# Optimization experiments

Hardware: AMD Instinct MI355X
Metric: run time of the kernel (lower is better)

## Reference

```python
import jax, jax.numpy as jnp
import numpy as np

N_NODES = 20000
N_EDGES = 8192
UNITS = 128
NUM_GAUSSIANS = 50
CUTOFF = 8.0
GAMMA = 10.0
MIN_DIST, MAX_DIST = 0.0, 30.0


def setup_inputs() -> dict:
    key = jax.random.key(0)
    ks = jax.random.split(key, 6)
    node_features = jax.random.normal(ks[0], (N_NODES, UNITS), dtype=jnp.float32)
    edge_indices = jax.random.randint(ks[1], (2, N_EDGES), 0, N_NODES, dtype=jnp.int32)
    distances = jax.random.uniform(ks[2], (N_EDGES,), dtype=jnp.float32)
    # filter network params (Dense(units) -> swish -> Dense(units*units))
    W1 = jax.random.normal(ks[3], (NUM_GAUSSIANS, UNITS), dtype=jnp.float32) / np.sqrt(NUM_GAUSSIANS)
    b1 = jnp.zeros((UNITS,), dtype=jnp.float32)
    W2 = jax.random.normal(ks[4], (UNITS, UNITS * UNITS), dtype=jnp.float32) / np.sqrt(UNITS)
    b2 = jnp.zeros((UNITS * UNITS,), dtype=jnp.float32)
    # transform Dense(units, use_bias=False)
    Wt = jax.random.normal(ks[5], (UNITS, UNITS), dtype=jnp.float32) / np.sqrt(UNITS)
    return {"node_features": node_features, "edge_indices": edge_indices,
            "distances": distances, "W1": W1, "b1": b1, "W2": W2, "b2": b2, "Wt": Wt}


def reference(node_features, edge_indices, distances, W1, b1, W2, b2, Wt):
    n_nodes, units = node_features.shape
    # cutoff mask (multiplicative; dropped edges contribute zero to the scatter-sum,
    # equivalent to tf.boolean_mask + unsorted_segment_sum)
    mask = (distances <= CUTOFF).astype(node_features.dtype)  # [E]
    # Gaussian basis expansion
    centers = jnp.linspace(MIN_DIST, MAX_DIST, NUM_GAUSSIANS, dtype=jnp.float32)
    df = jnp.exp(-GAMMA * jnp.square(distances[:, None] - centers[None, :]))  # [E, G]
    # filter network: Dense -> swish -> Dense(units*units)
    h = jax.nn.silu(df @ W1 + b1)                    # [E, U]
    filters = (h @ W2 + b2).reshape(-1, units, units)  # [E, U, U]
    # gather source node features, transform, per-edge matvec
    src = node_features[edge_indices[0]]             # [E, U]
    transformed = src @ Wt                           # [E, U]
    filtered = jnp.einsum('eij,ej->ei', filters, transformed) * mask[:, None]  # [E, U]
    # scatter-sum to destination nodes
    messages = jax.ops.segment_sum(filtered, edge_indices[1], num_segments=n_nodes)
    return jax.nn.silu(messages)
```

## Files before the change

kernel.cpp:

```cpp
#include <hip/hip_runtime.h>
#include <hip/hip_fp16.h>


typedef _Float16 f16;
typedef __attribute__((ext_vector_type(8))) f16 f16x8;
typedef __attribute__((ext_vector_type(4))) float f32x4;
typedef __attribute__((ext_vector_type(4))) unsigned int u32x4;

#define NEDGE 8192
#define NNODE 20000
#define NG    50
#define KSTEPS 516
#define W2C_BYTES (KSTEPS * 8192)
#define HT_ROWS 132
#define HT_BYTES (HT_ROWS * 8192 * 2)
#define TM_BYTES (NEDGE * 128 * 2)

#define LDS_H   0
#define LDS_TM  5120
#define LDS_B   37888
#define LDS_TOT 70656

static __device__ __forceinline__ float fsilu(float x) { return x / (1.0f + __expf(-x)); }

static __device__ __forceinline__ void gll16(const void* g, void* l) {
  __builtin_amdgcn_global_load_lds(
      (const __attribute__((address_space(1))) unsigned int*)g,
      (__attribute__((address_space(3))) unsigned int*)l, 16, 0, 0);
}

__global__ __launch_bounds__(256) void k0_w2c(const float* __restrict__ W2,
                                              const float* __restrict__ b2,
                                              f16* __restrict__ w2c) {
  int gidx = blockIdx.x * 256 + threadIdx.x;
  int lane = gidx & 63;
  int nt   = (gidx >> 6) & 7;
  int step = gidx >> 9;
  int k0i = step * 32 + (lane >> 4) * 8;
  int i   = nt * 16 + (lane & 15);
  int u   = k0i >> 7, j0 = k0i & 127;
  const float* src = (u < 128) ? (W2 + (size_t)u * 16384 + i * 128 + j0)
                               : (b2 + i * 128 + j0);
  union { f16 s[8]; u32x4 v; } pk;
#pragma unroll
  for (int r = 0; r < 8; ++r) pk.s[r] = (f16)src[r];
  *((u32x4*)w2c + gidx) = pk.v;
}

__global__ __launch_bounds__(256) void k1_edge(const float* __restrict__ NF,
                                               const int*   __restrict__ EI,
                                               const float* __restrict__ DI,
                                               const float* __restrict__ W1,
                                               const float* __restrict__ B1,
                                               const float* __restrict__ WT,
                                               f16* __restrict__ ht,
                                               f16* __restrict__ tmo) {
  __shared__ float df[16][NG];
  __shared__ float s_mask[16];
  __shared__ float s_src[16][128];
  __shared__ float t_tile[16][132];
  __shared__ float h_tile[16][132];
  int et = blockIdx.x, e0 = et * 16, tid = threadIdx.x;

  for (int idx = tid; idx < 16 * NG; idx += 256) {
    int e = idx / NG, g = idx - e * NG;
    float d = DI[e0 + e];
    float x = d - (float)g * (30.0f / 49.0f);
    df[e][g] = __expf(-10.0f * x * x);
  }
  if (tid < 16) s_mask[tid] = (DI[e0 + tid] <= 8.0f) ? 1.0f : 0.0f;
  for (int idx = tid; idx < 16 * 128; idx += 256) {
    int e = idx >> 7, u = idx & 127;
    s_src[e][u] = NF[(size_t)EI[e0 + e] * 128 + u];
  }
  __syncthreads();

  int j = tid & 127, es = tid >> 7;
  for (int e = es * 8; e < es * 8 + 8; ++e) {
    float acc = B1[j];
    for (int g = 0; g < NG; ++g) acc += df[e][g] * W1[g * 128 + j];
    h_tile[e][j] = fsilu(acc);
  }
  {
    float acc[8] = {0.f,0.f,0.f,0.f,0.f,0.f,0.f,0.f};
    for (int u = 0; u < 128; ++u) {
      float wv = WT[u * 128 + j];
#pragma unroll
      for (int e8 = 0; e8 < 8; ++e8) acc[e8] += s_src[es * 8 + e8][u] * wv;
    }
#pragma unroll
    for (int e8 = 0; e8 < 8; ++e8) t_tile[es * 8 + e8][j] = acc[e8];
  }
  __syncthreads();

  {
    int u = tid >> 1, hf = tid & 1;
    union { f16 s[8]; u32x4 v; } pk;
#pragma unroll
    for (int k = 0; k < 8; ++k) pk.s[k] = (f16)h_tile[hf * 8 + k][u];
    *(u32x4*)(ht + (size_t)u * 8192 + e0 + hf * 8) = pk.v;
  }
  if (tid < 16) ht[(size_t)128 * 8192 + e0 + tid] = (f16)1.0f;
  {
    int e = tid >> 4, cc = tid & 15;
    float m = s_mask[e];
    union { f16 s[8]; u32x4 v; } pk;
#pragma unroll
    for (int k = 0; k < 8; ++k) pk.s[k] = (f16)(m * t_tile[e][cc * 8 + k]);
    *(u32x4*)(tmo + (size_t)(e0 + e) * 128 + cc * 8) = pk.v;
  }
}

__global__ __launch_bounds__(256, 2) void k2_gemm(const f16* __restrict__ w2c,
                                                  const f16* __restrict__ ht,
                                                  const f16* __restrict__ tm,
                                                  const int* __restrict__ EI,
                                                  float* __restrict__ msg) {
  __shared__ u32x4 smem_v[LDS_TOT / 16];
  char* smem = (char*)smem_v;

  int bid = blockIdx.x;
  int c   = bid & 7;
  int eb  = bid >> 3;
  int e0  = eb * 128;
  int u0  = c * 16;
  int gstep0 = c * 64;
  int nsteps = (c == 7) ? 68 : 64;
  int tid = threadIdx.x, w = tid >> 6, lane = tid & 63;
  int l15 = lane & 15, g4 = lane >> 4;

  if (w == 0) {
#pragma unroll
    for (int q = 0; q < 5; ++q) {
      const char* src = (const char*)ht + ((size_t)(u0 + q * 4 + g4) * 8192 + e0 + l15 * 8) * 2;
      gll16(src, smem + LDS_H + q * 1024 + lane * 16);
    }
  }
#pragma unroll
  for (int it = 0; it < 8; ++it) {
    int ck = it * 256 + tid;
    int e = ck >> 4, jc = ck & 15;
    u32x4 v = *(const u32x4*)((const char*)tm + (size_t)(e0 + e) * 256 + jc * 16);
    *(u32x4*)(smem + LDS_TM + e * 256 + ((jc * 16) ^ ((e & 7) << 4))) = v;
  }
  const char* bsrc = (const char*)w2c + (size_t)gstep0 * 8192;
#pragma unroll
  for (int q = 0; q < 4; ++q)
    gll16(bsrc + w * 4096 + q * 1024 + lane * 16,
          smem + LDS_B + w * 4096 + q * 1024 + lane * 16);
  asm volatile("s_waitcnt vmcnt(0)" ::: "memory");
  __syncthreads();

  f32x4 acc[2][8];
#pragma unroll
  for (int rt = 0; rt < 2; ++rt)
#pragma unroll
    for (int nt = 0; nt < 8; ++nt) acc[rt][nt] = (f32x4){0.f, 0.f, 0.f, 0.f};

  __half2 hb0 = __half2half2(__half(0.f)), hb1 = hb0;
  const int tmswz = (l15 & 7) << 4;
  const int tma0  = LDS_TM + (w * 32 + l15) * 256;
  int nph = nsteps >> 1;

  for (int ph = 0; ph < nph; ++ph) {
    int cur = ph & 1;
    if (ph + 1 < nph) {
      const char* ns = bsrc + (size_t)(ph + 1) * 16384;
#pragma unroll
      for (int q = 0; q < 4; ++q)
        gll16(ns + w * 4096 + q * 1024 + lane * 16,
              smem + LDS_B + (1 - cur) * 16384 + w * 4096 + q * 1024 + lane * 16);
    }
    if ((ph & 1) == 0) {
      int uu = ph >> 1;
      const __half* hrow = (const __half*)(smem + LDS_H + uu * 256);
      hb0 = __half2half2(hrow[w * 32 + l15]);
      hb1 = __half2half2(hrow[w * 32 + 16 + l15]);
    }
#pragma unroll
    for (int s = 0; s < 2; ++s) {
      int s4 = ((ph & 1) << 1) | s;
      int coloff = (s4 * 64 + g4 * 16) ^ tmswz;
      union { f16x8 v; __half2 h2[4]; } t0, t1, a0, a1;
      t0.v = *(const f16x8*)(smem + tma0 + coloff);
      t1.v = *(const f16x8*)(smem + tma0 + 4096 + coloff);
#pragma unroll
      for (int q = 0; q < 4; ++q) {
        a0.h2[q] = __hmul2(t0.h2[q], hb0);
        a1.h2[q] = __hmul2(t1.h2[q], hb1);
      }
      const char* bb = smem + LDS_B + cur * 16384 + s * 8192 + lane * 16;
#pragma unroll
      for (int nt = 0; nt < 8; ++nt) {
        f16x8 b = *(const f16x8*)(bb + nt * 1024);
        acc[0][nt] = __builtin_amdgcn_mfma_f32_16x16x32_f16(a0.v, b, acc[0][nt], 0, 0, 0);
        acc[1][nt] = __builtin_amdgcn_mfma_f32_16x16x32_f16(a1.v, b, acc[1][nt], 0, 0, 0);
      }
    }
    asm volatile("s_waitcnt vmcnt(0)" ::: "memory");
    __syncthreads();
  }

  const int* dst = EI + NEDGE;
  int erow = e0 + w * 32;
#pragma unroll
  for (int rt = 0; rt < 2; ++rt)
#pragma unroll
    for (int r = 0; r < 4; ++r) {
      int e = erow + rt * 16 + g4 * 4 + r;
      float* row = msg + (size_t)dst[e] * 128 + l15;
#pragma unroll
      for (int nt = 0; nt < 8; ++nt)
        atomicAdd(row + nt * 16, acc[rt][nt][r]);
    }
}

__global__ __launch_bounds__(256) void k3_silu(float* __restrict__ out, int n4) {
  int idx = blockIdx.x * 256 + threadIdx.x;
  int stride = gridDim.x * 256;
  f32x4* p = (f32x4*)out;
  for (; idx < n4; idx += stride) {
    f32x4 v = p[idx];
#pragma unroll
    for (int cc = 0; cc < 4; ++cc) v[cc] = fsilu(v[cc]);
    p[idx] = v;
  }
}

extern "C" void kernel_launch(void* const* d_in, const int* in_sizes, int n_in,
                              void* d_out, int out_size, void* d_ws, size_t ws_size,
                              hipStream_t stream) {
  const float* NF = (const float*)d_in[0];
  const int*   EI = (const int*)  d_in[1];
  const float* DI = (const float*)d_in[2];
  const float* W1 = (const float*)d_in[3];
  const float* B1 = (const float*)d_in[4];
  const float* W2 = (const float*)d_in[5];
  const float* B2 = (const float*)d_in[6];
  const float* WT = (const float*)d_in[7];
  float* out = (float*)d_out;

  f16* w2c = (f16*)d_ws;
  f16* ht  = (f16*)((char*)d_ws + W2C_BYTES);
  f16* tmo = (f16*)((char*)d_ws + W2C_BYTES + HT_BYTES);
  size_t needed = (size_t)W2C_BYTES + HT_BYTES + TM_BYTES;
  if (ws_size < needed) return;

  hipMemsetAsync(d_out, 0, (size_t)out_size * sizeof(float), stream);
  k0_w2c <<<dim3(1032), dim3(256), 0, stream>>>(W2, B2, w2c);
  k1_edge<<<dim3(512),  dim3(256), 0, stream>>>(NF, EI, DI, W1, B1, WT, ht, tmo);
  k2_gemm<<<dim3(512),  dim3(256), 0, stream>>>(w2c, ht, tmo, EI, out);
  k3_silu<<<dim3(1024), dim3(256), 0, stream>>>(out, out_size / 4);
}
```

Baseline: 95.61 us.

## Restructure GEMM to 2x2 wave tiling with 4-stage B pipeline and pre-swizzled inputs

The edge kernel now writes the h matrix blocked per 128-edge tile and stores transformed features already XOR-swizzled, so the GEMM kernel can load both with direct global-to-LDS copies instead of register round-trips. The GEMM changes from a 1x4 wave layout (32 rows x 128 cols per wave) to a 2x2 layout (64x64 per wave), which cuts LDS reads per MFMA. It also replaces double buffering with a 4-slot ring and a partial vmcnt wait, so loads run further ahead without draining the queue each step. MFMA sections are wrapped in setprio. The deeper ring and larger A footprint raise register use, which may affect occupancy.

```diff
diff --git a/kernel.cpp b/kernel.cpp
--- a/kernel.cpp
+++ b/kernel.cpp
@@ -12,8 +12,7 @@
 #define NG    50
 #define KSTEPS 516
 #define W2C_BYTES (KSTEPS * 8192)
-#define HT_ROWS 132
-#define HT_BYTES (HT_ROWS * 8192 * 2)
+#define HT_BYTES (64 * 132 * 128 * 2)
 #define TM_BYTES (NEDGE * 128 * 2)
 
 #define LDS_H   0
@@ -53,7 +52,7 @@
                                                const float* __restrict__ W1,
                                                const float* __restrict__ B1,
                                                const float* __restrict__ WT,
-                                               f16* __restrict__ ht,
+                                               f16* __restrict__ ht2,
                                                f16* __restrict__ tmo) {
   __shared__ float df[16][NG];
   __shared__ float s_mask[16];
@@ -93,126 +92,130 @@
   }
   __syncthreads();
 
+  int eb = et >> 3, el0 = (et & 7) * 16;
   {
     int u = tid >> 1, hf = tid & 1;
     union { f16 s[8]; u32x4 v; } pk;
 #pragma unroll
     for (int k = 0; k < 8; ++k) pk.s[k] = (f16)h_tile[hf * 8 + k][u];
-    *(u32x4*)(ht + (size_t)u * 8192 + e0 + hf * 8) = pk.v;
-  }
-  if (tid < 16) ht[(size_t)128 * 8192 + e0 + tid] = (f16)1.0f;
+    *(u32x4*)(ht2 + ((size_t)eb * 132 + u) * 128 + el0 + hf * 8) = pk.v;
+  }
+  if (tid < 16) ht2[((size_t)eb * 132 + 128) * 128 + el0 + tid] = (f16)1.0f;
   {
     int e = tid >> 4, cc = tid & 15;
     float m = s_mask[e];
     union { f16 s[8]; u32x4 v; } pk;
 #pragma unroll
     for (int k = 0; k < 8; ++k) pk.s[k] = (f16)(m * t_tile[e][cc * 8 + k]);
-    *(u32x4*)(tmo + (size_t)(e0 + e) * 128 + cc * 8) = pk.v;
+    int col = (cc * 16) ^ ((e & 7) << 4);
+    *(u32x4*)((char*)tmo + (size_t)(e0 + e) * 256 + col) = pk.v;
   }
 }
 
 __global__ __launch_bounds__(256, 2) void k2_gemm(const f16* __restrict__ w2c,
-                                                  const f16* __restrict__ ht,
+                                                  const f16* __restrict__ ht2,
                                                   const f16* __restrict__ tm,
                                                   const int* __restrict__ EI,
                                                   float* __restrict__ msg) {
   __shared__ u32x4 smem_v[LDS_TOT / 16];
   char* smem = (char*)smem_v;
 
-  int bid = blockIdx.x;
-  int c   = bid & 7;
-  int eb  = bid >> 3;
-  int e0  = eb * 128;
-  int u0  = c * 16;
-  int gstep0 = c * 64;
-  int nsteps = (c == 7) ? 68 : 64;
-  int tid = threadIdx.x, w = tid >> 6, lane = tid & 63;
-  int l15 = lane & 15, g4 = lane >> 4;
-
+  const int bid = blockIdx.x;
+  const int c   = bid & 7;
+  const int eb  = bid >> 3;
+  const int e0  = eb * 128;
+  const int nu  = (c == 7) ? 17 : 16;
+  const int nph = nu * 4;
+  const int tid = threadIdx.x, w = tid >> 6, lane = tid & 63;
+  const int l15 = lane & 15, g4 = lane >> 4;
+  const int wm = w >> 1, wn = w & 1;
+
+  const char* bsrc = (const char*)w2c + (size_t)(c * 64) * 8192;
+
+  {
+    const char* tsrc = (const char*)tm + (size_t)e0 * 256 + w * 8192;
+#pragma unroll
+    for (int q = 0; q < 8; ++q)
+      gll16(tsrc + q * 1024 + lane * 16,
+            smem + LDS_TM + w * 8192 + q * 1024 + lane * 16);
+  }
   if (w == 0) {
-#pragma unroll
-    for (int q = 0; q < 5; ++q) {
-      const char* src = (const char*)ht + ((size_t)(u0 + q * 4 + g4) * 8192 + e0 + l15 * 8) * 2;
-      gll16(src, smem + LDS_H + q * 1024 + lane * 16);
+    const char* hsrc = (const char*)ht2 + ((size_t)eb * 132 + c * 16) * 256;
+#pragma unroll
+    for (int q = 0; q < 5; ++q)
+      gll16(hsrc + q * 1024 + lane * 16, smem + LDS_H + q * 1024 + lane * 16);
+  }
+#pragma unroll
+  for (int q = 0; q < 2; ++q)
+    gll16(bsrc + w * 2048 + q * 1024 + lane * 16,
+          smem + LDS_B + w * 2048 + q * 1024 + lane * 16);
+#pragma unroll
+  for (int q = 0; q < 2; ++q)
+    gll16(bsrc + 8192 + w * 2048 + q * 1024 + lane * 16,
+          smem + LDS_B + 8192 + w * 2048 + q * 1024 + lane * 16);
+  asm volatile("s_waitcnt vmcnt(2)" ::: "memory");
+  __builtin_amdgcn_s_barrier();
+
+  f32x4 acc[4][4];
+#pragma unroll
+  for (int rt = 0; rt < 4; ++rt)
+#pragma unroll
+    for (int nt = 0; nt < 4; ++nt) acc[rt][nt] = (f32x4){0.f, 0.f, 0.f, 0.f};
+
+  const int tmbase = LDS_TM + (wm * 64 + l15) * 256;
+  const int colsw  = (l15 & 7) << 4;
+  const int bcol   = wn * 4096 + lane * 16;
+  const __half* hbase = (const __half*)(smem + LDS_H) + wm * 64 + l15;
+
+  for (int u = 0; u < nu; ++u) {
+    __half2 h2[4];
+#pragma unroll
+    for (int rt = 0; rt < 4; ++rt) h2[rt] = __half2half2(hbase[u * 128 + rt * 16]);
+#pragma unroll
+    for (int jc = 0; jc < 4; ++jc) {
+      const int p = u * 4 + jc;
+      int ps = p + 2; ps = (ps < nph) ? ps : (nph - 1);
+      const char* ns = bsrc + (size_t)ps * 8192 + w * 2048;
+      char* nd = smem + LDS_B + ((jc + 2) & 3) * 8192 + w * 2048;
+      gll16(ns + lane * 16, nd + lane * 16);
+      gll16(ns + 1024 + lane * 16, nd + 1024 + lane * 16);
+      union uf { f16x8 v; __half2 h[4]; };
+      uf a[4];
+#pragma unroll
+      for (int rt = 0; rt < 4; ++rt) {
+        uf t;
+        t.v = *(const f16x8*)(smem + tmbase + rt * 4096 + ((jc * 64 + g4 * 16) ^ colsw));
+#pragma unroll
+        for (int q = 0; q < 4; ++q) a[rt].h[q] = __hmul2(t.h[q], h2[rt]);
+      }
+      f16x8 b[4];
+#pragma unroll
+      for (int nt = 0; nt < 4; ++nt)
+        b[nt] = *(const f16x8*)(smem + LDS_B + jc * 8192 + bcol + nt * 1024);
+      __builtin_amdgcn_s_setprio(1);
+#pragma unroll
+      for (int nt = 0; nt < 4; ++nt)
+#pragma unroll
+        for (int rt = 0; rt < 4; ++rt)
+          acc[rt][nt] = __builtin_amdgcn_mfma_f32_16x16x32_f16(a[rt].v, b[nt], acc[rt][nt], 0, 0, 0);
+      __builtin_amdgcn_s_setprio(0);
+      asm volatile("s_waitcnt vmcnt(2)" ::: "memory");
+      __builtin_amdgcn_s_barrier();
     }
   }
-#pragma unroll
-  for (int it = 0; it < 8; ++it) {
-    int ck = it * 256 + tid;
-    int e = ck >> 4, jc = ck & 15;
-    u32x4 v = *(const u32x4*)((const char*)tm + (size_t)(e0 + e) * 256 + jc * 16);
-    *(u32x4*)(smem + LDS_TM + e * 256 + ((jc * 16) ^ ((e & 7) << 4))) = v;
-  }
-  const char* bsrc = (const char*)w2c + (size_t)gstep0 * 8192;
-#pragma unroll
-  for (int q = 0; q < 4; ++q)
-    gll16(bsrc + w * 4096 + q * 1024 + lane * 16,
-          smem + LDS_B + w * 4096 + q * 1024 + lane * 16);
-  asm volatile("s_waitcnt vmcnt(0)" ::: "memory");
-  __syncthreads();
-
-  f32x4 acc[2][8];
-#pragma unroll
-  for (int rt = 0; rt < 2; ++rt)
-#pragma unroll
-    for (int nt = 0; nt < 8; ++nt) acc[rt][nt] = (f32x4){0.f, 0.f, 0.f, 0.f};
-
-  __half2 hb0 = __half2half2(__half(0.f)), hb1 = hb0;
-  const int tmswz = (l15 & 7) << 4;
-  const int tma0  = LDS_TM + (w * 32 + l15) * 256;
-  int nph = nsteps >> 1;
-
-  for (int ph = 0; ph < nph; ++ph) {
-    int cur = ph & 1;
-    if (ph + 1 < nph) {
-      const char* ns = bsrc + (size_t)(ph + 1) * 16384;
-#pragma unroll
-      for (int q = 0; q < 4; ++q)
-        gll16(ns + w * 4096 + q * 1024 + lane * 16,
-              smem + LDS_B + (1 - cur) * 16384 + w * 4096 + q * 1024 + lane * 16);
-    }
-    if ((ph & 1) == 0) {
-      int uu = ph >> 1;
-      const __half* hrow = (const __half*)(smem + LDS_H + uu * 256);
-      hb0 = __half2half2(hrow[w * 32 + l15]);
-      hb1 = __half2half2(hrow[w * 32 + 16 + l15]);
-    }
-#pragma unroll
-    for (int s = 0; s < 2; ++s) {
-      int s4 = ((ph & 1) << 1) | s;
-      int coloff = (s4 * 64 + g4 * 16) ^ tmswz;
-      union { f16x8 v; __half2 h2[4]; } t0, t1, a0, a1;
-      t0.v = *(const f16x8*)(smem + tma0 + coloff);
-      t1.v = *(const f16x8*)(smem + tma0 + 4096 + coloff);
-#pragma unroll
-      for (int q = 0; q < 4; ++q) {
-        a0.h2[q] = __hmul2(t0.h2[q], hb0);
-        a1.h2[q] = __hmul2(t1.h2[q], hb1);
-      }
-      const char* bb = smem + LDS_B + cur * 16384 + s * 8192 + lane * 16;
-#pragma unroll
-      for (int nt = 0; nt < 8; ++nt) {
-        f16x8 b = *(const f16x8*)(bb + nt * 1024);
-        acc[0][nt] = __builtin_amdgcn_mfma_f32_16x16x32_f16(a0.v, b, acc[0][nt], 0, 0, 0);
-        acc[1][nt] = __builtin_amdgcn_mfma_f32_16x16x32_f16(a1.v, b, acc[1][nt], 0, 0, 0);
-      }
-    }
-    asm volatile("s_waitcnt vmcnt(0)" ::: "memory");
-    __syncthreads();
-  }
 
   const int* dst = EI + NEDGE;
-  int erow = e0 + w * 32;
-#pragma unroll
-  for (int rt = 0; rt < 2; ++rt)
+#pragma unroll
+  for (int rt = 0; rt < 4; ++rt) {
 #pragma unroll
     for (int r = 0; r < 4; ++r) {
-      int e = erow + rt * 16 + g4 * 4 + r;
-      float* row = msg + (size_t)dst[e] * 128 + l15;
-#pragma unroll
-      for (int nt = 0; nt < 8; ++nt)
+      int e = e0 + wm * 64 + rt * 16 + g4 * 4 + r;
+      float* row = msg + (size_t)dst[e] * 128 + wn * 64 + l15;
+#pragma unroll
+      for (int nt = 0; nt < 4; ++nt)
         atomicAdd(row + nt * 16, acc[rt][nt][r]);
     }
+  }
 }
 
 __global__ __launch_bounds__(256) void k3_silu(float* __restrict__ out, int n4) {
@@ -241,14 +244,14 @@
   float* out = (float*)d_out;
 
   f16* w2c = (f16*)d_ws;
-  f16* ht  = (f16*)((char*)d_ws + W2C_BYTES);
+  f16* ht2 = (f16*)((char*)d_ws + W2C_BYTES);
   f16* tmo = (f16*)((char*)d_ws + W2C_BYTES + HT_BYTES);
   size_t needed = (size_t)W2C_BYTES + HT_BYTES + TM_BYTES;
   if (ws_size < needed) return;
 
   hipMemsetAsync(d_out, 0, (size_t)out_size * sizeof(float), stream);
   k0_w2c <<<dim3(1032), dim3(256), 0, stream>>>(W2, B2, w2c);
-  k1_edge<<<dim3(512),  dim3(256), 0, stream>>>(NF, EI, DI, W1, B1, WT, ht, tmo);
-  k2_gemm<<<dim3(512),  dim3(256), 0, stream>>>(w2c, ht, tmo, EI, out);
+  k1_edge<<<dim3(512),  dim3(256), 0, stream>>>(NF, EI, DI, W1, B1, WT, ht2, tmo);
+  k2_gemm<<<dim3(512),  dim3(256), 0, stream>>>(w2c, ht2, tmo, EI, out);
   k3_silu<<<dim3(1024), dim3(256), 0, stream>>>(out, out_size / 4);
 }
```

Result: no change. 96.60 us (+1.0%).
